# Kernel tuning notes

Measured on AMD Instinct MI355X. Metric: run time of the kernel, lower is better.

## Reference

```python
import jax, jax.numpy as jnp
import numpy as np

B, IMG, P, NP, S = 16, 224, 16, 196, 197
D, H, DH, L, FF = 768, 12, 64, 12, 3072


def setup_inputs() -> dict:
    key = jax.random.key(0)
    ks = jax.random.split(key, 16)
    nrm = lambda k, shape: jax.random.normal(k, shape, jnp.float32) * 0.02
    return {
        "x": jax.random.normal(ks[0], (B, IMG, IMG, 3), jnp.float32),
        "cls": jnp.zeros((1, 1, D), jnp.float32),
        "pos_emb": nrm(ks[1], (S, D)),
        "Wp": nrm(ks[2], (P * P * 3, D)), "bp": jnp.zeros((D,), jnp.float32),
        "Wq": nrm(ks[3], (L, D, D)), "bq": jnp.zeros((L, D), jnp.float32),
        "Wk": nrm(ks[4], (L, D, D)), "bk": jnp.zeros((L, D), jnp.float32),
        "Wv": nrm(ks[5], (L, D, D)), "bv": jnp.zeros((L, D), jnp.float32),
        "Wo": nrm(ks[6], (L, D, D)), "bo": jnp.zeros((L, D), jnp.float32),
        "ln1g": jnp.ones((L, D), jnp.float32), "ln1b": jnp.zeros((L, D), jnp.float32),
        "ln2g": jnp.ones((L, D), jnp.float32), "ln2b": jnp.zeros((L, D), jnp.float32),
        "W1": nrm(ks[7], (L, D, FF)), "b1": jnp.zeros((L, FF), jnp.float32),
        "W2": nrm(ks[8], (L, FF, D)), "b2": jnp.zeros((L, D), jnp.float32),
        "lnfg": jnp.ones((D,), jnp.float32), "lnfb": jnp.zeros((D,), jnp.float32),
    }


def _ln(y, g, b, eps):
    m = y.mean(-1, keepdims=True)
    v = ((y - m) ** 2).mean(-1, keepdims=True)
    return (y - m) / jnp.sqrt(v + eps) * g + b


def _gelu(z):
    # tanh-approx GeLU, exactly as in the source module
    return 0.5 * z * (1.0 + jnp.tanh(np.sqrt(2.0 / np.pi) * (z + 0.044715 * z ** 3)))


def reference(x, cls, pos_emb, Wp, bp, Wq, bq, Wk, bk, Wv, bv, Wo, bo,
              ln1g, ln1b, ln2g, ln2b, W1, b1, W2, b2, lnfg, lnfb):
    Bb = x.shape[0]
    g = IMG // P  # 14 patches per side
    # tf.image.extract_patches with VALID, stride==size: row-major patch flatten
    patches = x.reshape(Bb, g, P, g, P, 3).transpose(0, 1, 3, 2, 4, 5).reshape(Bb, NP, P * P * 3)
    h = patches @ Wp + bp                               # [B, 196, D]
    h = jnp.concatenate([jnp.broadcast_to(cls, (Bb, 1, D)), h], axis=1) + pos_emb  # [B, S, D]

    scale = np.float32(1.0 / np.sqrt(DH))

    def block(h, p):
        wq, bq_, wk, bk_, wv, bv_, wo, bo_, g1, gb1, g2, gb2, w1, b1_, w2, b2_ = p
        y = _ln(h, g1, gb1, 1e-6)
        q = (y @ wq + bq_).reshape(Bb, S, H, DH).transpose(0, 2, 1, 3)  # [B,H,S,dh]
        k = (y @ wk + bk_).reshape(Bb, S, H, DH).transpose(0, 2, 1, 3)
        v = (y @ wv + bv_).reshape(Bb, S, H, DH).transpose(0, 2, 1, 3)
        w = jax.nn.softmax(jnp.einsum('bhqd,bhkd->bhqk', q, k) * scale, axis=-1)
        att = jnp.einsum('bhqk,bhkd->bhqd', w, v)       # [B,H,S,dh]
        # NOTE: in the source the two Permutes cancel, so the "concat" is a raw
        # reshape of the [B,H,S,dh] tensor to [B,S,D] (heads interleaved). Faithful.
        concat = att.reshape(Bb, S, D)
        h1 = h + concat @ wo + bo_
        y = _ln(h1, g2, gb2, 1e-6)
        y = _gelu(y @ w1 + b1_) @ w2 + b2_
        return h1 + y, None

    h, _ = jax.lax.scan(block, h, (Wq, bq, Wk, bk, Wv, bv, Wo, bo,
                                   ln1g, ln1b, ln2g, ln2b, W1, b1, W2, b2))
    return _ln(h, lnfg, lnfb, 1e-3)  # final Keras LayerNorm, default eps=1e-3
```

## Files before the change

### kernel.cpp

```cpp
#include <hip/hip_runtime.h>
#include <cstdint>
#include <cstddef>

#define DD   768
#define HHN  12
#define SS   197
#define FFD  3072
#define MROWS 3152
#define MPAD  3200
#define PROWS 3136
#define PSTRIDE 2457600

typedef __attribute__((ext_vector_type(4))) float  f32x4;
typedef __attribute__((ext_vector_type(8))) __bf16 bf16x8;
typedef __attribute__((ext_vector_type(4))) __bf16 bf16x4;

__global__ __launch_bounds__(256) void w2ball_k(
    const float* __restrict__ Wp, const float* __restrict__ Wq, const float* __restrict__ Wk,
    const float* __restrict__ Wv, const float* __restrict__ Wo, const float* __restrict__ W1,
    const float* __restrict__ W2,
    __bf16* __restrict__ Wpb, __bf16* __restrict__ Wqb, __bf16* __restrict__ Wkb,
    __bf16* __restrict__ Wvb, __bf16* __restrict__ Wob, __bf16* __restrict__ W1b,
    __bf16* __restrict__ W2b)
{
  const int bidx = blockIdx.x;
  const float* W; __bf16* Wb; int NT, loc;
  if      (bidx <    72) { W = Wp; Wb = Wpb; NT =  3; loc = bidx;        }
  else if (bidx <   936) { W = Wq; Wb = Wqb; NT =  3; loc = bidx - 72;   }
  else if (bidx <  1800) { W = Wk; Wb = Wkb; NT =  3; loc = bidx - 936;  }
  else if (bidx <  2664) { W = Wv; Wb = Wvb; NT =  3; loc = bidx - 1800; }
  else if (bidx <  3528) { W = Wo; Wb = Wob; NT =  3; loc = bidx - 2664; }
  else if (bidx <  6984) { W = W1; Wb = W1b; NT = 12; loc = bidx - 3528; }
  else                   { W = W2; Wb = W2b; NT =  3; loc = bidx - 6984; }
  const int N  = NT * 256;
  const int n0 = (loc % NT) * 256, k0 = (loc / NT) * 32;

  const int t  = threadIdx.x;
  const int kg = t >> 6;
  const int n  = n0 + (t & 63) * 4;

  const int kb = k0 + kg * 8;
  f32x4 v[8];
  #pragma unroll
  for (int j = 0; j < 8; ++j)
    v[j] = *(const f32x4*)(W + (size_t)(kb + j) * N + n);

  __bf16* out = Wb + ((size_t)((k0 >> 3) + kg) * N + n) * 8;
  #pragma unroll
  for (int c = 0; c < 4; ++c) {
    bf16x8 o;
    #pragma unroll
    for (int j = 0; j < 8; ++j) o[j] = (__bf16)v[j][c];
    *(bf16x8*)(out + c * 8) = o;
  }
}

template<int BN, int NMAT, int MODE, bool GELU_, bool STOREBF, bool VT>
__global__ __launch_bounds__(256) void gemm_k(
    const __bf16* __restrict__ A,
    const __bf16* __restrict__ Bb0, const __bf16* __restrict__ Bb1, const __bf16* __restrict__ Bb2,
    const float* __restrict__ bias0, const float* __restrict__ bias1, const float* __restrict__ bias2,
    float* __restrict__ Cf, __bf16* __restrict__ Cb, __bf16* __restrict__ vt,
    int N, int Kloc, int Kstride)
{
  const int xcd = blockIdx.x & 7;
  const int ib  = blockIdx.x >> 3;
  const int NT  = N / BN;
  const int pm  = xcd >> 1, pn = xcd & 1;
  const int cm  = 6 + (pm < 1 ? 1 : 0);
  const int bm  = pm * 6 + (pm < 1 ? pm : 1);
  const int cn  = NT >> 1;
  if (ib >= cm * cn) return;
  const int mt  = bm + ib % cm;
  const int nt  = pn * cn + ib / cm;
  const int m0  = mt * 128;
  const int n0  = nt * BN;
  const int kz  = blockIdx.y;
  const size_t kOff = (size_t)kz * Kloc;

  constexpr int BUFB = (BN == 128) ? 16384 : 12288;
  __shared__ char lds[3 * BUFB];
  const int tid = threadIdx.x;

  int mat = 0, nB = n0, NBw = N;
  const __bf16* Bbp = Bb0; const float* biasp = bias0;
  if (NMAT == 3) {
    mat = n0 / DD; nB = n0 - mat * DD; NBw = DD;
    Bbp   = (mat == 0) ? Bb0   : ((mat == 1) ? Bb1   : Bb2);
    biasp = (mat == 0) ? bias0 : ((mat == 1) ? bias1 : bias2);
  }

  constexpr int NC = (BN == 128) ? 4 : 2;
  f32x4 acc[4][NC];
  const f32x4 z4 = {0.f, 0.f, 0.f, 0.f};
  #pragma unroll
  for (int i = 0; i < 4; ++i)
    #pragma unroll
    for (int j = 0; j < NC; ++j) acc[i][j] = z4;

  const int lane = tid & 63;
  const int wv = tid >> 6;
  const int wr = wv >> 1, wc = wv & 1;
  const int arow = tid & 127, akh = tid >> 7;

  const int nKB = Kloc >> 5;

  auto issue = [&](int kt, int buf) {
    const int k0 = kt << 5;
    char* Ab = lds + buf * BUFB;
    char* Bbl = Ab + 8192;
    {
      const __bf16* ga0 = A + (size_t)(m0 + arow) * Kstride + kOff + k0 + akh * 8;
      auto g0 = (__attribute__((address_space(1))) unsigned int*)(uintptr_t)ga0;
      auto g1 = (__attribute__((address_space(1))) unsigned int*)(uintptr_t)(ga0 + 16);
      auto l0 = (__attribute__((address_space(3))) unsigned int*)(uintptr_t)(Ab + wv * 1024);
      auto l1 = (__attribute__((address_space(3))) unsigned int*)(uintptr_t)(Ab + 4096 + wv * 1024);
      __builtin_amdgcn_global_load_lds(g0, l0, 16, 0, 0);
      __builtin_amdgcn_global_load_lds(g1, l1, 16, 0, 0);
    }
    if (BN == 128) {
      #pragma unroll
      for (int r = 0; r < 2; ++r) {
        const int c = r * 256 + tid;
        const int g = c >> 7, col = c & 127;
        const __bf16* gb = Bbp + ((size_t)(((kOff + k0) >> 3) + g) * NBw + nB + col) * 8;
        auto gp = (__attribute__((address_space(1))) unsigned int*)(uintptr_t)gb;
        auto lp = (__attribute__((address_space(3))) unsigned int*)(uintptr_t)(Bbl + r * 4096 + wv * 1024);
        __builtin_amdgcn_global_load_lds(gp, lp, 16, 0, 0);
      }
    } else {
      const __bf16* gb = Bbp + ((size_t)(((kOff + k0) >> 3) + wv) * NBw + nB + lane) * 8;
      auto gp = (__attribute__((address_space(1))) unsigned int*)(uintptr_t)gb;
      auto lp = (__attribute__((address_space(3))) unsigned int*)(uintptr_t)(Bbl + wv * 1024);
      __builtin_amdgcn_global_load_lds(gp, lp, 16, 0, 0);
    }
  };

  constexpr int WAITIMM = (BN == 128) ? 0xF78  : 0xF76 ;

  issue(0, 0);
  issue(nKB > 1 ? 1 : 0, 1);

  int cb = 0, wb = 2;
  const int q = lane >> 4, r16 = lane & 15;
  for (int kb = 0; kb < nKB; ++kb) {
    __builtin_amdgcn_sched_barrier(0);
    __builtin_amdgcn_s_barrier();
    const int nxt = kb + 2;
    issue(nxt < nKB ? nxt : nKB - 1, wb);
    __builtin_amdgcn_s_waitcnt(WAITIMM);
    __builtin_amdgcn_s_barrier();
    __builtin_amdgcn_sched_barrier(0);

    const char* Ab = lds + cb * BUFB;
    const char* Bbl = Ab + 8192;
    const char* pa = Ab + q * 2048 + (wr * 64 + r16) * 16;
    const char* pb = (BN == 128) ? (Bbl + q * 2048 + (wc * 64 + r16) * 16)
                                 : (Bbl + q * 1024 + (wc * 32 + r16) * 16);
    bf16x8 af[4], bfv[NC];
    #pragma unroll
    for (int i = 0; i < 4; ++i) af[i]  = *(const bf16x8*)(pa + i * 256);
    #pragma unroll
    for (int i = 0; i < NC; ++i) bfv[i] = *(const bf16x8*)(pb + i * 256);
    #pragma unroll
    for (int ri = 0; ri < 4; ++ri)
      #pragma unroll
      for (int ci = 0; ci < NC; ++ci)
        acc[ri][ci] = __builtin_amdgcn_mfma_f32_16x16x32_bf16(af[ri], bfv[ci], acc[ri][ci], 0, 0, 0);

    cb = (cb == 2) ? 0 : cb + 1;
    wb = (wb == 2) ? 0 : wb + 1;
  }
  __builtin_amdgcn_s_waitcnt(0);

  const int q4 = (lane >> 4) * 4, c16 = lane & 15;
  #pragma unroll
  for (int ci = 0; ci < NC; ++ci) {
    const int n = n0 + ((BN == 128) ? wc * 64 : wc * 32) + ci * 16 + c16;
    const float bsv = ((MODE == 1 || MODE == 2) && kz != 0) ? 0.f
                      : biasp[(NMAT == 3) ? (n - mat * DD) : n];
    #pragma unroll
    for (int ri = 0; ri < 4; ++ri) {
      const int mb = m0 + wr * 64 + ri * 16 + q4;
      #pragma unroll
      for (int rg = 0; rg < 4; ++rg) {
        float v = acc[ri][ci][rg] + bsv;
        const int row = mb + rg;
        if (VT && NMAT == 3 && mat == 2) {
          const int b = row / SS;
          if (b < 16) {
            const int s = row - b * SS;
            const int nloc = n - 2 * DD;
            const int hh = nloc >> 6, d = nloc & 63;
            vt[((size_t)(b * HHN + hh) * 28 + (s >> 3)) * 512 + d * 8 + (s & 7)] = (__bf16)v;
          }
        } else {
          const size_t off = (size_t)row * N + n;
          if (MODE == 1) {
            atomicAdd(&Cf[off], v);
          } else if (MODE == 2) {
            Cf[(size_t)kz * PSTRIDE + off] = v;
          } else {
            if (GELU_) {
              const float zz = v;
              const float a = 0.7978845608028654f * (zz + 0.044715f * zz * zz * zz);
              v = 0.5f * zz * (2.0f - 2.0f / (1.0f + __expf(2.0f * a)));
            }
            if (STOREBF) Cb[off] = (__bf16)v; else Cf[off] = v;
          }
        }
      }
    }
  }
}

__global__ __launch_bounds__(256) void attn_k(const __bf16* __restrict__ qkv,
                                              const __bf16* __restrict__ vt,
                                              __bf16* __restrict__ att)
{
  __shared__ char als[58240];
  const int t = threadIdx.x;
  const int qt = blockIdx.x, bh = blockIdx.y;
  const int b = bh / HHN, hh = bh % HHN;
  const int r0 = qt * 64;

  bf16x8 vstage[7];
  #pragma unroll
  for (int i = 0; i < 7; ++i)
    vstage[i] = *(const bf16x8*)(vt + (size_t)bh * 14336 + (size_t)(t + i * 256) * 8);

  #pragma unroll
  for (int i = 0; i < 7; ++i) {
    const int c = t + i * 256;
    const int kh = c & 7, s = c >> 3;
    const int sg = s < SS ? s : (SS - 1);
    const bf16x8 v = *(const bf16x8*)(qkv + (size_t)(b * SS + sg) * 2304 + DD + hh * 64 + kh * 8);
    *(bf16x8*)(als + kh * 3600 + s * 16) = v;
  }
  #pragma unroll
  for (int i = 0; i < 2; ++i) {
    const int c = t + i * 256;
    const int qr = c & 63, dh8 = c >> 6;
    const int rr = r0 + qr;
    const int sg = rr < SS ? rr : (SS - 1);
    const bf16x8 v = *(const bf16x8*)(qkv + (size_t)(b * SS + sg) * 2304 + hh * 64 + dh8 * 8);
    *(bf16x8*)(als + 28800 + dh8 * 1040 + qr * 16) = v;
  }
  __syncthreads();

  const int w = t >> 6, lane = t & 63;
  const int q = lane >> 4, c16 = lane & 15;
  const f32x4 z4 = {0.f, 0.f, 0.f, 0.f};

  f32x4 acc[13];
  #pragma unroll
  for (int nt = 0; nt < 13; ++nt) acc[nt] = z4;
  #pragma unroll
  for (int kk = 0; kk < 2; ++kk) {
    const bf16x8 af = *(const bf16x8*)(als + 28800 + (kk * 4 + q) * 1040 + (w * 16 + c16) * 16);
    #pragma unroll
    for (int nt = 0; nt < 13; ++nt) {
      const bf16x8 bf_ = *(const bf16x8*)(als + (kk * 4 + q) * 3600 + (nt * 16 + c16) * 16);
      acc[nt] = __builtin_amdgcn_mfma_f32_16x16x32_bf16(af, bf_, acc[nt], 0, 0, 0);
    }
  }
  __syncthreads();

  float inv[4];
  #pragma unroll
  for (int rg = 0; rg < 4; ++rg) {
    float mx = -1e30f;
    #pragma unroll
    for (int nt = 0; nt < 13; ++nt) {
      const bool val = (nt < 12) || (c16 < 5);
      const float sv = acc[nt][rg] * 0.125f;
      if (val) mx = fmaxf(mx, sv);
    }
    #pragma unroll
    for (int m = 1; m < 16; m <<= 1) mx = fmaxf(mx, __shfl_xor(mx, m, 16));
    float sm = 0.f;
    #pragma unroll
    for (int nt = 0; nt < 13; ++nt) {
      const bool val = (nt < 12) || (c16 < 5);
      const float e = val ? __expf(acc[nt][rg] * 0.125f - mx) : 0.f;
      acc[nt][rg] = e; sm += e;
    }
    #pragma unroll
    for (int m = 1; m < 16; m <<= 1) sm += __shfl_xor(sm, m, 16);
    inv[rg] = 1.f / sm;
  }

  #pragma unroll
  for (int nt = 0; nt < 14; ++nt) {
    #pragma unroll
    for (int rg = 0; rg < 4; ++rg) {
      const int s = nt * 16 + c16;
      const int qr = w * 16 + q * 4 + rg;
      const float pv = (nt < 13) ? acc[nt][rg] * inv[rg] : 0.f;
      *(__bf16*)(als + (s >> 3) * 1040 + qr * 16 + (s & 7) * 2) = (__bf16)pv;
    }
  }
  #pragma unroll
  for (int i = 0; i < 7; ++i) {
    const int c = t + i * 256;
    *(bf16x8*)(als + 29120 + (c >> 6) * 1040 + (c & 63) * 16) = vstage[i];
  }
  __syncthreads();

  f32x4 o[4];
  #pragma unroll
  for (int dt = 0; dt < 4; ++dt) o[dt] = z4;
  #pragma unroll
  for (int kk = 0; kk < 7; ++kk) {
    const bf16x8 af = *(const bf16x8*)(als + (kk * 4 + q) * 1040 + (w * 16 + c16) * 16);
    #pragma unroll
    for (int dt = 0; dt < 4; ++dt) {
      const bf16x8 bf_ = *(const bf16x8*)(als + 29120 + (kk * 4 + q) * 1040 + (dt * 16 + c16) * 16);
      o[dt] = __builtin_amdgcn_mfma_f32_16x16x32_bf16(af, bf_, o[dt], 0, 0, 0);
    }
  }
  #pragma unroll
  for (int dt = 0; dt < 4; ++dt) {
    #pragma unroll
    for (int rg = 0; rg < 4; ++rg) {
      const int r = r0 + w * 16 + q * 4 + rg;
      if (r < SS)
        att[((size_t)bh * SS + r) * 64 + dt * 16 + c16] = (__bf16)o[dt][rg];
    }
  }
}

template<bool OUTBF>
__global__ __launch_bounds__(256) void ln_k(const float* __restrict__ X,
    const float* __restrict__ g, const float* __restrict__ be, float eps,
    __bf16* __restrict__ Yb, float* __restrict__ Yf)
{
  const int row = blockIdx.x * 4 + (threadIdx.x >> 6), l = threadIdx.x & 63;
  const f32x4* xr = (const f32x4*)(X + (size_t)row * DD);
  f32x4 v[3];
  #pragma unroll
  for (int j = 0; j < 3; ++j) v[j] = xr[l + j * 64];
  float s = 0.f;
  #pragma unroll
  for (int j = 0; j < 3; ++j) s += v[j][0] + v[j][1] + v[j][2] + v[j][3];
  #pragma unroll
  for (int m = 1; m < 64; m <<= 1) s += __shfl_xor(s, m, 64);
  const float mean = s * (1.f / 768.f);
  float vs = 0.f;
  #pragma unroll
  for (int j = 0; j < 3; ++j)
    #pragma unroll
    for (int e = 0; e < 4; ++e) { const float d = v[j][e] - mean; vs += d * d; }
  #pragma unroll
  for (int m = 1; m < 64; m <<= 1) vs += __shfl_xor(vs, m, 64);
  const float rstd = rsqrtf(vs * (1.f / 768.f) + eps);
  const f32x4* gp = (const f32x4*)g; const f32x4* bp = (const f32x4*)be;
  #pragma unroll
  for (int j = 0; j < 3; ++j) {
    const int c4 = l + j * 64;
    const f32x4 gg = gp[c4], bb = bp[c4];
    if (OUTBF) {
      bf16x4 o;
      #pragma unroll
      for (int e = 0; e < 4; ++e) o[e] = (__bf16)((v[j][e] - mean) * rstd * gg[e] + bb[e]);
      *(bf16x4*)(Yb + (size_t)row * DD + c4 * 4) = o;
    } else {
      f32x4 o;
      #pragma unroll
      for (int e = 0; e < 4; ++e) o[e] = (v[j][e] - mean) * rstd * gg[e] + bb[e];
      *(f32x4*)(Yf + (size_t)row * DD + c4 * 4) = o;
    }
  }
}

template<int NPART, bool OUTBF, bool WRITEH>
__global__ __launch_bounds__(256) void lnsum_k(const float* X,
    const float* __restrict__ P, const float* __restrict__ g, const float* __restrict__ be,
    float eps, __bf16* __restrict__ Yb, float* __restrict__ Yf, float* Hout)
{
  const int row = blockIdx.x * 4 + (threadIdx.x >> 6), l = threadIdx.x & 63;
  const f32x4* xr = (const f32x4*)(X + (size_t)row * DD);
  f32x4 v[3];
  #pragma unroll
  for (int j = 0; j < 3; ++j) v[j] = xr[l + j * 64];
  #pragma unroll
  for (int p = 0; p < NPART; ++p) {
    const f32x4* pr = (const f32x4*)(P + (size_t)p * PSTRIDE + (size_t)row * DD);
    #pragma unroll
    for (int j = 0; j < 3; ++j) v[j] += pr[l + j * 64];
  }
  if (WRITEH) {
    f32x4* hw = (f32x4*)(Hout + (size_t)row * DD);
    #pragma unroll
    for (int j = 0; j < 3; ++j) hw[l + j * 64] = v[j];
  }
  float s = 0.f;
  #pragma unroll
  for (int j = 0; j < 3; ++j) s += v[j][0] + v[j][1] + v[j][2] + v[j][3];
  #pragma unroll
  for (int m = 1; m < 64; m <<= 1) s += __shfl_xor(s, m, 64);
  const float mean = s * (1.f / 768.f);
  float vs = 0.f;
  #pragma unroll
  for (int j = 0; j < 3; ++j)
    #pragma unroll
    for (int e = 0; e < 4; ++e) { const float d = v[j][e] - mean; vs += d * d; }
  #pragma unroll
  for (int m = 1; m < 64; m <<= 1) vs += __shfl_xor(vs, m, 64);
  const float rstd = rsqrtf(vs * (1.f / 768.f) + eps);
  const f32x4* gp = (const f32x4*)g; const f32x4* bp = (const f32x4*)be;
  #pragma unroll
  for (int j = 0; j < 3; ++j) {
    const int c4 = l + j * 64;
    const f32x4 gg = gp[c4], bb = bp[c4];
    if (OUTBF) {
      bf16x4 o;
      #pragma unroll
      for (int e = 0; e < 4; ++e) o[e] = (__bf16)((v[j][e] - mean) * rstd * gg[e] + bb[e]);
      *(bf16x4*)(Yb + (size_t)row * DD + c4 * 4) = o;
    } else {
      f32x4 o;
      #pragma unroll
      for (int e = 0; e < 4; ++e) o[e] = (v[j][e] - mean) * rstd * gg[e] + bb[e];
      *(f32x4*)(Yf + (size_t)row * DD + c4 * 4) = o;
    }
  }
}

__global__ __launch_bounds__(256) void im2col_k(const float* __restrict__ x, __bf16* __restrict__ patches)
{
  const int idx = blockIdx.x * 256 + threadIdx.x;
  const int row = idx / 48, col0 = (idx % 48) * 16;
  if (row < PROWS) {
    const int b = row / 196, p = row % 196;
    const int py = p / 14, px = p % 14;
    const int r = col0 / 48, o = col0 % 48;
    const float* src = x + ((size_t)(b * 224 + py * 16 + r) * 224 + px * 16) * 3 + o;
    f32x4 v[4];
    #pragma unroll
    for (int j = 0; j < 4; ++j) v[j] = *(const f32x4*)(src + j * 4);
    bf16x8 o0, o1;
    #pragma unroll
    for (int e = 0; e < 8; ++e) { o0[e] = (__bf16)v[e >> 2][e & 3]; o1[e] = (__bf16)v[2 + (e >> 2)][e & 3]; }
    *(bf16x8*)(patches + (size_t)row * 768 + col0)     = o0;
    *(bf16x8*)(patches + (size_t)row * 768 + col0 + 8) = o1;
  } else if (row < MPAD) {
    const bf16x8 z = {};
    *(bf16x8*)(patches + (size_t)row * 768 + col0)     = z;
    *(bf16x8*)(patches + (size_t)row * 768 + col0 + 8) = z;
  }
}

__global__ __launch_bounds__(256) void assemble_k(const float* __restrict__ tmp, const float* __restrict__ cls,
    const float* __restrict__ pos, float* __restrict__ h)
{
  const int idx = blockIdx.x * 256 + threadIdx.x;
  const int row = idx / 192, qc = (idx % 192) * 4;
  f32x4 v = {0.f, 0.f, 0.f, 0.f};
  if (row < MROWS) {
    const int b = row / SS, s2 = row % SS;
    if (s2 == 0) v = *(const f32x4*)(cls + qc);
    else         v = *(const f32x4*)(tmp + (size_t)(b * 196 + s2 - 1) * 768 + qc);
    const f32x4 p = *(const f32x4*)(pos + (size_t)s2 * 768 + qc);
    v += p;
  }
  *(f32x4*)(h + (size_t)row * 768 + qc) = v;
}

extern "C" void kernel_launch(void* const* d_in, const int* in_sizes, int n_in,
                              void* d_out, int out_size, void* d_ws, size_t ws_size,
                              hipStream_t stream)
{
  (void)in_sizes; (void)n_in; (void)out_size;
  const float* x    = (const float*)d_in[0];
  const float* cls  = (const float*)d_in[1];
  const float* pos  = (const float*)d_in[2];
  const float* Wp   = (const float*)d_in[3];
  const float* bp   = (const float*)d_in[4];
  const float* Wq   = (const float*)d_in[5];
  const float* bq   = (const float*)d_in[6];
  const float* Wk   = (const float*)d_in[7];
  const float* bk   = (const float*)d_in[8];
  const float* Wv   = (const float*)d_in[9];
  const float* bv   = (const float*)d_in[10];
  const float* Wo   = (const float*)d_in[11];
  const float* bo   = (const float*)d_in[12];
  const float* ln1g = (const float*)d_in[13];
  const float* ln1b = (const float*)d_in[14];
  const float* ln2g = (const float*)d_in[15];
  const float* ln2b = (const float*)d_in[16];
  const float* W1   = (const float*)d_in[17];
  const float* b1   = (const float*)d_in[18];
  const float* W2   = (const float*)d_in[19];
  const float* b2   = (const float*)d_in[20];
  const float* lnfg = (const float*)d_in[21];
  const float* lnfb = (const float*)d_in[22];

  char* ws = (char*)d_ws;
  float*  h    = (float*) (ws + 0);
  __bf16* y    = (__bf16*)(ws + 9830400);
  __bf16* qkv  = (__bf16*)(ws + 14745600);
  float*  tmp  = (float*) (ws + 14745600);
  __bf16* att  = (__bf16*)(ws + 29491200);
  __bf16* mffn = (__bf16*)(ws + 34406400);
  __bf16* patches = (__bf16*)(ws + 34406400);
  __bf16* Wpb = (__bf16*)(ws + 54067200);
  __bf16* Wqb = (__bf16*)(ws + 55246848);
  __bf16* Wkb = (__bf16*)(ws + 69402624);
  __bf16* Wvb = (__bf16*)(ws + 83558400);
  __bf16* Wob = (__bf16*)(ws + 97714176);
  __bf16* W1b = (__bf16*)(ws + 111869952);
  __bf16* W2b = (__bf16*)(ws + 168493056);
  __bf16* vt  = (__bf16*)(ws + 225116160);
  float*  pbuf = (float*)(ws + 230621184);
  if (ws_size < 269942784) return;

  w2ball_k<<<10440, 256, 0, stream>>>(Wp, Wq, Wk, Wv, Wo, W1, W2,
                                      Wpb, Wqb, Wkb, Wvb, Wob, W1b, W2b);

  im2col_k<<<MPAD * 48 / 256, 256, 0, stream>>>(x, patches);
  gemm_k<64,1,2,false,false,false><<<12*32, 256, 0, stream>>>(
      patches, Wpb,Wpb,Wpb, bp,bp,bp, tmp, nullptr, nullptr, DD, DD, DD);
  assemble_k<<<MPAD * 192 / 256, 256, 0, stream>>>(tmp, cls, pos, h);

  ln_k<true><<<MROWS / 4, 256, 0, stream>>>(h, ln1g, ln1b, 1e-6f, y, nullptr);
  for (int l = 0; l < 12; ++l) {
    const size_t wDD = (size_t)l * DD * DD, wFF = (size_t)l * DD * FFD;
    gemm_k<128,3,0,false,true,true><<<18*32, 256, 0, stream>>>(
        y, Wqb + wDD, Wkb + wDD, Wvb + wDD,
        bq + l*DD, bk + l*DD, bv + l*DD, nullptr, qkv, vt, 3*DD, DD, DD);
    attn_k<<<dim3(4, 192), 256, 0, stream>>>(qkv, vt, att);
    gemm_k<64,1,2,false,false,false><<<dim3(12*32, 2), 256, 0, stream>>>(
        att, Wob + wDD, nullptr, nullptr, bo + l*DD, nullptr, nullptr,
        pbuf, nullptr, nullptr, DD, DD/2, DD);
    lnsum_k<2,true,true><<<MROWS / 4, 256, 0, stream>>>(
        h, pbuf, ln2g + l*DD, ln2b + l*DD, 1e-6f, y, nullptr, h);
    gemm_k<128,1,0,true,true,false><<<24*32, 256, 0, stream>>>(
        y, W1b + wFF, nullptr, nullptr, b1 + l*FFD, nullptr, nullptr,
        nullptr, mffn, nullptr, FFD, DD, DD);
    gemm_k<128,1,2,false,false,false><<<dim3(6*32, 4), 256, 0, stream>>>(
        mffn, W2b + wFF, nullptr, nullptr, b2 + l*DD, nullptr, nullptr,
        pbuf, nullptr, nullptr, DD, FFD/4, FFD);
    if (l < 11)
      lnsum_k<4,true,true><<<MROWS / 4, 256, 0, stream>>>(
          h, pbuf, ln1g + (l+1)*DD, ln1b + (l+1)*DD, 1e-6f, y, nullptr, h);
  }
  lnsum_k<4,false,false><<<MROWS / 4, 256, 0, stream>>>(
      h, pbuf, lnfg, lnfb, 1e-3f, nullptr, (float*)d_out, nullptr);
}
```

Before: 2.231 ms.

## Overlap next-layer weight bf16 conversion with current-layer GEMMs via extra blocks

```diff
diff --git a/kernel.cpp b/kernel.cpp
--- a/kernel.cpp
+++ b/kernel.cpp
@@ -15,7 +15,31 @@
 typedef __attribute__((ext_vector_type(8))) __bf16 bf16x8;
 typedef __attribute__((ext_vector_type(4))) __bf16 bf16x4;
 
-__global__ __launch_bounds__(256) void w2ball_k(
+__device__ __forceinline__ void conv_tile(const float* __restrict__ W,
+                                          __bf16* __restrict__ Wb,
+                                          int NT, int loc)
+{
+  const int N  = NT * 256;
+  const int n0 = (loc % NT) * 256, k0 = (loc / NT) * 32;
+  const int t  = threadIdx.x;
+  const int kg = t >> 6;
+  const int n  = n0 + (t & 63) * 4;
+  const int kb = k0 + kg * 8;
+  f32x4 v[8];
+  #pragma unroll
+  for (int j = 0; j < 8; ++j)
+    v[j] = *(const f32x4*)(W + (size_t)(kb + j) * N + n);
+  __bf16* out = Wb + ((size_t)((k0 >> 3) + kg) * N + n) * 8;
+  #pragma unroll
+  for (int c = 0; c < 4; ++c) {
+    bf16x8 o;
+    #pragma unroll
+    for (int j = 0; j < 8; ++j) o[j] = (__bf16)v[j][c];
+    *(bf16x8*)(out + c * 8) = o;
+  }
+}
+
+__global__ __launch_bounds__(256) void w2binit_k(
     const float* __restrict__ Wp, const float* __restrict__ Wq, const float* __restrict__ Wk,
     const float* __restrict__ Wv, const float* __restrict__ Wo, const float* __restrict__ W1,
     const float* __restrict__ W2,
@@ -24,35 +48,13 @@
     __bf16* __restrict__ W2b)
 {
   const int bidx = blockIdx.x;
-  const float* W; __bf16* Wb; int NT, loc;
-  if      (bidx <    72) { W = Wp; Wb = Wpb; NT =  3; loc = bidx;        }
-  else if (bidx <   936) { W = Wq; Wb = Wqb; NT =  3; loc = bidx - 72;   }
-  else if (bidx <  1800) { W = Wk; Wb = Wkb; NT =  3; loc = bidx - 936;  }
-  else if (bidx <  2664) { W = Wv; Wb = Wvb; NT =  3; loc = bidx - 1800; }
-  else if (bidx <  3528) { W = Wo; Wb = Wob; NT =  3; loc = bidx - 2664; }
-  else if (bidx <  6984) { W = W1; Wb = W1b; NT = 12; loc = bidx - 3528; }
-  else                   { W = W2; Wb = W2b; NT =  3; loc = bidx - 6984; }
-  const int N  = NT * 256;
-  const int n0 = (loc % NT) * 256, k0 = (loc / NT) * 32;
-
-  const int t  = threadIdx.x;
-  const int kg = t >> 6;
-  const int n  = n0 + (t & 63) * 4;
-
-  const int kb = k0 + kg * 8;
-  f32x4 v[8];
-  #pragma unroll
-  for (int j = 0; j < 8; ++j)
-    v[j] = *(const f32x4*)(W + (size_t)(kb + j) * N + n);
-
-  __bf16* out = Wb + ((size_t)((k0 >> 3) + kg) * N + n) * 8;
-  #pragma unroll
-  for (int c = 0; c < 4; ++c) {
-    bf16x8 o;
-    #pragma unroll
-    for (int j = 0; j < 8; ++j) o[j] = (__bf16)v[j][c];
-    *(bf16x8*)(out + c * 8) = o;
-  }
+  if      (bidx <  72) conv_tile(Wp, Wpb,  3, bidx);
+  else if (bidx < 144) conv_tile(Wq, Wqb,  3, bidx - 72);
+  else if (bidx < 216) conv_tile(Wk, Wkb,  3, bidx - 144);
+  else if (bidx < 288) conv_tile(Wv, Wvb,  3, bidx - 216);
+  else if (bidx < 360) conv_tile(Wo, Wob,  3, bidx - 288);
+  else if (bidx < 648) conv_tile(W1, W1b, 12, bidx - 360);
+  else                 conv_tile(W2, W2b,  3, bidx - 648);
 }
 
 template<int BN, int NMAT, int MODE, bool GELU_, bool STOREBF, bool VT>
@@ -61,8 +63,22 @@
     const __bf16* __restrict__ Bb0, const __bf16* __restrict__ Bb1, const __bf16* __restrict__ Bb2,
     const float* __restrict__ bias0, const float* __restrict__ bias1, const float* __restrict__ bias2,
     float* __restrict__ Cf, __bf16* __restrict__ Cb, __bf16* __restrict__ vt,
-    int N, int Kloc, int Kstride)
-{
+    int N, int Kloc, int Kstride,
+    const float* cS0, const float* cS1, const float* cS2,
+    __bf16* cD0, __bf16* cD1, __bf16* cD2,
+    int cNT, int cPer, int cBlocks)
+{
+  const int gemmGrid = (int)gridDim.x - cBlocks;
+  if ((int)blockIdx.x >= gemmGrid) {
+    if (blockIdx.y == 0) {
+      const int cl = (int)blockIdx.x - gemmGrid;
+      const int mi = cl / cPer, li = cl - mi * cPer;
+      conv_tile(mi == 0 ? cS0 : (mi == 1 ? cS1 : cS2),
+                mi == 0 ? cD0 : (mi == 1 ? cD1 : cD2), cNT, li);
+    }
+    return;
+  }
+
   const int xcd = blockIdx.x & 7;
   const int ib  = blockIdx.x >> 3;
   const int NT  = N / BN;
@@ -515,32 +531,48 @@
   float*  pbuf = (float*)(ws + 230621184);
   if (ws_size < 269942784) return;
 
-  w2ball_k<<<10440, 256, 0, stream>>>(Wp, Wq, Wk, Wv, Wo, W1, W2,
-                                      Wpb, Wqb, Wkb, Wvb, Wob, W1b, W2b);
+  w2binit_k<<<936, 256, 0, stream>>>(Wp, Wq, Wk, Wv, Wo, W1, W2,
+                                     Wpb, Wqb, Wkb, Wvb, Wob, W1b, W2b);
 
   im2col_k<<<MPAD * 48 / 256, 256, 0, stream>>>(x, patches);
   gemm_k<64,1,2,false,false,false><<<12*32, 256, 0, stream>>>(
-      patches, Wpb,Wpb,Wpb, bp,bp,bp, tmp, nullptr, nullptr, DD, DD, DD);
+      patches, Wpb,Wpb,Wpb, bp,bp,bp, tmp, nullptr, nullptr, DD, DD, DD,
+      nullptr,nullptr,nullptr, nullptr,nullptr,nullptr, 1, 1, 0);
   assemble_k<<<MPAD * 192 / 256, 256, 0, stream>>>(tmp, cls, pos, h);
 
   ln_k<true><<<MROWS / 4, 256, 0, stream>>>(h, ln1g, ln1b, 1e-6f, y, nullptr);
   for (int l = 0; l < 12; ++l) {
     const size_t wDD = (size_t)l * DD * DD, wFF = (size_t)l * DD * FFD;
-    gemm_k<128,3,0,false,true,true><<<18*32, 256, 0, stream>>>(
+    const bool cv = (l < 11);
+    const size_t nDD = (size_t)(l + 1) * DD * DD, nFF = (size_t)(l + 1) * DD * FFD;
+
+    gemm_k<128,3,0,false,true,true><<<dim3(18*32 + (cv ? 216 : 0)), 256, 0, stream>>>(
         y, Wqb + wDD, Wkb + wDD, Wvb + wDD,
-        bq + l*DD, bk + l*DD, bv + l*DD, nullptr, qkv, vt, 3*DD, DD, DD);
+        bq + l*DD, bk + l*DD, bv + l*DD, nullptr, qkv, vt, 3*DD, DD, DD,
+        cv ? Wq + nDD : nullptr, cv ? Wk + nDD : nullptr, cv ? Wv + nDD : nullptr,
+        cv ? Wqb + nDD : nullptr, cv ? Wkb + nDD : nullptr, cv ? Wvb + nDD : nullptr,
+        3, 72, cv ? 216 : 0);
     attn_k<<<dim3(4, 192), 256, 0, stream>>>(qkv, vt, att);
-    gemm_k<64,1,2,false,false,false><<<dim3(12*32, 2), 256, 0, stream>>>(
+    gemm_k<64,1,2,false,false,false><<<dim3(12*32 + (cv ? 72 : 0), 2), 256, 0, stream>>>(
         att, Wob + wDD, nullptr, nullptr, bo + l*DD, nullptr, nullptr,
-        pbuf, nullptr, nullptr, DD, DD/2, DD);
+        pbuf, nullptr, nullptr, DD, DD/2, DD,
+        cv ? Wo + nDD : nullptr, nullptr, nullptr,
+        cv ? Wob + nDD : nullptr, nullptr, nullptr,
+        3, 72, cv ? 72 : 0);
     lnsum_k<2,true,true><<<MROWS / 4, 256, 0, stream>>>(
         h, pbuf, ln2g + l*DD, ln2b + l*DD, 1e-6f, y, nullptr, h);
-    gemm_k<128,1,0,true,true,false><<<24*32, 256, 0, stream>>>(
+    gemm_k<128,1,0,true,true,false><<<dim3(24*32 + (cv ? 288 : 0)), 256, 0, stream>>>(
         y, W1b + wFF, nullptr, nullptr, b1 + l*FFD, nullptr, nullptr,
-        nullptr, mffn, nullptr, FFD, DD, DD);
-    gemm_k<128,1,2,false,false,false><<<dim3(6*32, 4), 256, 0, stream>>>(
+        nullptr, mffn, nullptr, FFD, DD, DD,
+        cv ? W1 + nFF : nullptr, nullptr, nullptr,
+        cv ? W1b + nFF : nullptr, nullptr, nullptr,
+        12, 288, cv ? 288 : 0);
+    gemm_k<128,1,2,false,false,false><<<dim3(6*32 + (cv ? 288 : 0), 4), 256, 0, stream>>>(
         mffn, W2b + wFF, nullptr, nullptr, b2 + l*DD, nullptr, nullptr,
-        pbuf, nullptr, nullptr, DD, FFD/4, FFD);
+        pbuf, nullptr, nullptr, DD, FFD/4, FFD,
+        cv ? W2 + nFF : nullptr, nullptr, nullptr,
+        cv ? W2b + nFF : nullptr, nullptr, nullptr,
+        3, 288, cv ? 288 : 0);
     if (l < 11)
       lnsum_k<4,true,true><<<MROWS / 4, 256, 0, stream>>>(
           h, pbuf, ln1g + (l+1)*DD, ln1b + (l+1)*DD, 1e-6f, y, nullptr, h);
```

Measured after the change: 2.159 ms. 3.3% less time.
